# Kernel optimization log

Measured on AMD Instinct MI355X. Metric: run time of the kernel, lower is better.

The kernel has to match this reference:

```python
import jax, jax.numpy as jnp
import numpy as np

SCALE = 10.0
KB = 1.0  # kernel_bandwidth

B, D, P, M, K = 128, 128, 4, 100000, 10


def _sqdist(a, b):
    # a: [..., N, D], b: [..., M, D] -> squared euclidean [..., N, M]
    a2 = jnp.sum(a * a, axis=-1)[..., :, None]
    b2 = jnp.sum(b * b, axis=-1)[..., None, :]
    ab = jnp.einsum('...nd,...md->...nm', a, b)
    return jnp.maximum(a2 + b2 - 2.0 * ab, 0.0)


def setup_inputs() -> dict:
    key = jax.random.key(0)
    k1, k2, k3, k4, k5, k6, k7 = jax.random.split(key, 7)
    return {
        'global_img_feat': jax.random.normal(k1, (B, D), jnp.float32),
        'global_text_feat': jax.random.normal(k2, (B, D), jnp.float32),
        'local_img_feats': jax.random.normal(k3, (P, B, D), jnp.float32),
        'centers': jax.random.normal(k4, (P, M, D), jnp.float32),
        'cross_indices': jax.random.randint(k5, (B, K), 0, M, jnp.int64),
        'position': jax.random.randint(k6, (B,), 0, M, jnp.int64),
        'memory_vid': jax.random.randint(k7, (M,), 0, 1000, jnp.int64),
    }


def reference(global_img_feat, global_text_feat, local_img_feats, centers,
              cross_indices, position, memory_vid):
    b = global_img_feat.shape[0]
    # ---- global MMD alignment (text branch detached) ----
    img = global_img_feat / jnp.linalg.norm(global_img_feat, axis=1, keepdims=True)
    txt_d = jax.lax.stop_gradient(global_text_feat)
    txt = txt_d / jnp.linalg.norm(txt_d, axis=1, keepdims=True)
    inv2kb2 = 1.0 / (2.0 * KB * KB)
    k_xx = jnp.exp(-_sqdist(img, img) * inv2kb2)
    k_yy = jnp.exp(-_sqdist(txt, txt) * inv2kb2)
    k_xy = jnp.exp(-_sqdist(img, txt) * inv2kb2)
    off = ~jnp.eye(b, dtype=bool)
    denom = b * (b - 1)
    mmd = (jnp.sum(jnp.where(off, k_xx, 0.0)) / denom
           + jnp.sum(jnp.where(off, k_yy, 0.0)) / denom
           - 2.0 * jnp.mean(k_xy))
    # ---- local part contrastive loss (vectorized over P parts) ----
    m = centers.shape[1]
    pos_feat = centers[:, cross_indices]                       # [P,B,K,D]
    f2 = jnp.sum(local_img_feats ** 2, axis=-1)                # [P,B]
    p2 = jnp.sum(pos_feat ** 2, axis=-1)                       # [P,B,K]
    fp = jnp.einsum('pbd,pbkd->pbk', local_img_feats, pos_feat)
    pos_dist = jnp.sqrt(jnp.maximum(f2[..., None] + p2 - 2.0 * fp, 0.0))  # [P,B,K]
    neg_dist = jnp.sqrt(_sqdist(local_img_feats, centers))     # [P,B,M]
    # negative mask over memory slots (int indices are constants)
    neg_mask = jnp.ones((m,), bool).at[cross_indices.reshape(-1)].set(False)
    neg_mask = neg_mask.at[position].set(False)
    x = jnp.log(jnp.sum(jnp.exp(-SCALE * pos_dist), axis=-1))  # [P,B]
    y = jnp.log(jnp.sum(jnp.exp(-SCALE * neg_dist) * neg_mask[None, None, :], axis=-1))
    l = jnp.sum(-x + y, axis=1) / local_img_feats.shape[1]     # [P]
    l = jnp.where(jnp.isnan(l), 0.0, l)
    local_loss = jnp.sum(l) / local_img_feats.shape[0]
    total = local_loss + 1.0 * mmd
    pos_vid = memory_vid[cross_indices]                        # [B,K]
    return total, local_loss, mmd, pos_vid
```

## Files before the change

kernel.cpp:

```cpp
#include <hip/hip_runtime.h>
#include <math.h>

#define B_ 128
#define D_ 128
#define P_ 4
#define M_ 100000
#define K_ 10
#define SCALE_ 10.0f
#define MB_ 782
#define NEG_BLOCKS (MB_ * P_)
#define MMD_BLOCKS 128
#define POS_BLOCKS 128
#define D2_CUT 120.0f

typedef short bf16x8 __attribute__((ext_vector_type(8)));
typedef float floatx4 __attribute__((ext_vector_type(4)));

__device__ inline unsigned pack_bf16_trunc(unsigned f0, unsigned f1) {
    return __builtin_amdgcn_perm(f1, f0, 0x07060302u);
}

template <int CTRL>
__device__ inline float dpp_add(float v) {
    int x = __builtin_amdgcn_update_dpp(0, __builtin_bit_cast(int, v), CTRL, 0xF, 0xF, true);
    return v + __builtin_bit_cast(float, x);
}
__device__ inline float row16Sum(float v) {
    v = dpp_add<0xB1>(v);
    v = dpp_add<0x4E>(v);
    v = dpp_add<0x141>(v);
    v = dpp_add<0x140>(v);
    return v;
}
__device__ inline float waveSum64(float v) {
    v = row16Sum(v);
    v += __shfl_xor(v, 16, 64);
    v += __shfl_xor(v, 32, 64);
    return v;
}
__device__ inline float waveReduceSumOld(float v) {
    #pragma unroll
    for (int off = 32; off > 0; off >>= 1) v += __shfl_xor(v, off, 64);
    return v;
}
__device__ inline float blockReduce128(float v, float* sh2) {
    v = waveSum64(v);
    int wid = threadIdx.x >> 6;
    if ((threadIdx.x & 63) == 0) sh2[wid] = v;
    __syncthreads();
    float r = sh2[0] + sh2[1];
    __syncthreads();
    return r;
}

__global__ __launch_bounds__(128) void k_prep(const float* __restrict__ img,
                                              const float* __restrict__ txt,
                                              const float* __restrict__ local,
                                              float* imgT, float* txtT,
                                              float* a2i, float* a2t,
                                              float* f2w, float* s_neg) {
    __shared__ float sh2[2];
    int bid = blockIdx.x, t = threadIdx.x;
    if (bid < 256) {
        int row = bid & 127, which = bid >> 7;
        if (bid < 4) s_neg[bid * 128 + t] = 0.f;
        const float* src = which ? txt : img;
        float* dstT = which ? txtT : imgT;
        float* a2 = which ? a2t : a2i;
        float v = src[row * D_ + t];
        float s = blockReduce128(v * v, sh2);
        float n = v / sqrtf(s);
        dstT[t * 128 + row] = n;
        float s2 = blockReduce128(n * n, sh2);
        if (t == 0) a2[row] = s2;
    } else {
        int r = bid - 256;
        float v = local[(size_t)r * D_ + t];
        float s = blockReduce128(v * v, sh2);
        if (t == 0) f2w[r] = s;
    }
}

__global__ __launch_bounds__(256, 3) void k_main(const float* __restrict__ local,
                                                 const float* __restrict__ centers,
                                                 const float* __restrict__ imgT,
                                                 const float* __restrict__ txtT,
                                                 const float* __restrict__ a2i,
                                                 const float* __restrict__ a2t,
                                                 const int* __restrict__ ci,
                                                 const int* __restrict__ posi,
                                                 const int* __restrict__ mvid,
                                                 const float* __restrict__ f2w,
                                                 float* __restrict__ s_neg,
                                                 float* __restrict__ s_pos,
                                                 double* __restrict__ mmd_part,
                                                 float* __restrict__ out) {
    union Smem {
        struct {
            bf16x8 A_lds[2048];
            float sred[512];
            float f2l[128];
            unsigned char msk[128];
        } n;
        struct {
            float ri[128], rt[128];
            float sh2[2];
        } m;
    };
    __shared__ Smem sm;
    const int bid = blockIdx.x;
    const int t = threadIdx.x;
    const int w = t >> 6;
    const int l = t & 63;

    if (bid < NEG_BLOCKS) {
        const int p = bid / MB_;
        const int mb = bid - p * MB_;
        const int m0 = mb * 128;
        const int n16 = l & 15;
        const int q = l >> 4;

        const float* lp = local + (size_t)p * B_ * D_;
        if (t < 128) { sm.n.msk[t] = 1; sm.n.f2l[t] = f2w[p * 128 + t]; }
        #pragma unroll
        for (int s8 = 0; s8 < 8; s8++) {
            int f = t + 256 * s8;
            int fl = f & 63, bt = (f >> 6) & 7, kc = f >> 9;
            int row = bt * 16 + (fl & 15);
            int col = kc * 32 + ((fl >> 4) & 3) * 8;
            const uint4 u0 = *(const uint4*)(lp + row * D_ + col);
            const uint4 u1 = *(const uint4*)(lp + row * D_ + col + 4);
            union { bf16x8 v; unsigned u[4]; } fr;
            fr.u[0] = pack_bf16_trunc(u0.x, u0.y);
            fr.u[1] = pack_bf16_trunc(u0.z, u0.w);
            fr.u[2] = pack_bf16_trunc(u1.x, u1.y);
            fr.u[3] = pack_bf16_trunc(u1.z, u1.w);
            sm.n.A_lds[f] = fr.v;
        }
        __syncthreads();

        int gm[2];
        gm[0] = m0 + (w * 2 + 0) * 16 + n16;
        gm[1] = m0 + (w * 2 + 1) * 16 + n16;
        const float* cb = centers + (size_t)p * M_ * D_;
        uint4 rb[2][4][2];
        if (m0 + 128 <= M_) {
            #pragma unroll
            for (int wm = 0; wm < 2; wm++) {
                const uint4* src = (const uint4*)(cb + (size_t)gm[wm] * D_ + q * 8);
                #pragma unroll
                for (int kc = 0; kc < 4; kc++) {
                    rb[wm][kc][0] = src[kc * 8];
                    rb[wm][kc][1] = src[kc * 8 + 1];
                }
            }
        } else {
            const uint4 z = make_uint4(0u, 0u, 0u, 0u);
            #pragma unroll
            for (int wm = 0; wm < 2; wm++) {
                const uint4* src = (const uint4*)(cb + (size_t)gm[wm] * D_ + q * 8);
                #pragma unroll
                for (int kc = 0; kc < 4; kc++) {
                    if (gm[wm] < M_) {
                        rb[wm][kc][0] = src[kc * 8];
                        rb[wm][kc][1] = src[kc * 8 + 1];
                    } else {
                        rb[wm][kc][0] = z;
                        rb[wm][kc][1] = z;
                    }
                }
            }
        }

        #pragma unroll
        for (int i = 0; i < 5; i++) {
            int idx = ci[t + 256 * i];
            unsigned r = (unsigned)(idx - m0);
            if (r < 128u) sm.n.msk[r] = 0;
        }
        if (t < B_) {
            unsigned r = (unsigned)(posi[t] - m0);
            if (r < 128u) sm.n.msk[r] = 0;
        }
        __syncthreads();

        float c2a[2];
        bf16x8 bfr[2][4];
        #pragma unroll
        for (int wm = 0; wm < 2; wm++) {
            float c = 0.f;
            #pragma unroll
            for (int kc = 0; kc < 4; kc++) {
                union { uint4 u; floatx4 f; } a, b;
                a.u = rb[wm][kc][0];
                b.u = rb[wm][kc][1];
                c += a.f[0]*a.f[0] + a.f[1]*a.f[1] + a.f[2]*a.f[2] + a.f[3]*a.f[3]
                   + b.f[0]*b.f[0] + b.f[1]*b.f[1] + b.f[2]*b.f[2] + b.f[3]*b.f[3];
                union { bf16x8 v; unsigned u[4]; } fr;
                fr.u[0] = pack_bf16_trunc(a.u.x, a.u.y);
                fr.u[1] = pack_bf16_trunc(a.u.z, a.u.w);
                fr.u[2] = pack_bf16_trunc(b.u.x, b.u.y);
                fr.u[3] = pack_bf16_trunc(b.u.z, b.u.w);
                bfr[wm][kc] = fr.v;
            }
            c2a[wm] = c;
        }

        floatx4 acc[8][2];
        #pragma unroll
        for (int bt = 0; bt < 8; bt++) { acc[bt][0] = (floatx4)(0.f); acc[bt][1] = (floatx4)(0.f); }
        #pragma unroll
        for (int kc = 0; kc < 4; kc++) {
            #pragma unroll
            for (int bt = 0; bt < 8; bt++) {
                bf16x8 af = sm.n.A_lds[kc * 512 + bt * 64 + l];
                acc[bt][0] = __builtin_amdgcn_mfma_f32_16x16x32_bf16(af, bfr[0][kc], acc[bt][0], 0, 0, 0);
                acc[bt][1] = __builtin_amdgcn_mfma_f32_16x16x32_bf16(af, bfr[1][kc], acc[bt][1], 0, 0, 0);
            }
        }

        float c2v[2];
        #pragma unroll
        for (int wm = 0; wm < 2; wm++) {
            float c = c2a[wm];
            c += __shfl_xor(c, 16, 64);
            c += __shfl_xor(c, 32, 64);
            c2v[wm] = c;
        }

        float dmin = 1e30f;
        #pragma unroll
        for (int bt = 0; bt < 8; bt++) {
            floatx4 f4 = *(const floatx4*)&sm.n.f2l[bt * 16 + q * 4];
            #pragma unroll
            for (int r = 0; r < 4; r++) {
                float d20 = fmaf(-2.f, acc[bt][0][r], f4[r] + c2v[0]);
                float d21 = fmaf(-2.f, acc[bt][1][r], f4[r] + c2v[1]);
                dmin = fminf(dmin, fminf(d20, d21));
            }
        }
        if (!__any(dmin < D2_CUT)) {
            sm.n.sred[w * 128 + l] = 0.f;
            sm.n.sred[w * 128 + l + 64] = 0.f;
        } else {
            float vm0 = (gm[0] < M_ && sm.n.msk[(w * 2 + 0) * 16 + n16] != 0) ? 1.f : 0.f;
            float vm1 = (gm[1] < M_ && sm.n.msk[(w * 2 + 1) * 16 + n16] != 0) ? 1.f : 0.f;
            #pragma unroll
            for (int bt = 0; bt < 8; bt++) {
                floatx4 f4 = *(const floatx4*)&sm.n.f2l[bt * 16 + q * 4];
                #pragma unroll
                for (int r = 0; r < 4; r++) {
                    float s = 0.f;
                    float d20 = fmaxf(fmaf(-2.f, acc[bt][0][r], f4[r] + c2v[0]), 0.f);
                    float d21 = fmaxf(fmaf(-2.f, acc[bt][1][r], f4[r] + c2v[1]), 0.f);
                    if (d20 < D2_CUT) s += vm0 * expf(-SCALE_ * sqrtf(d20));
                    if (d21 < D2_CUT) s += vm1 * expf(-SCALE_ * sqrtf(d21));
                    s = row16Sum(s);
                    if (n16 == 0) sm.n.sred[w * 128 + bt * 16 + q * 4 + r] = s;
                }
            }
        }
        __syncthreads();
        if (t < 128) {
            float s = sm.n.sred[t] + sm.n.sred[128 + t] + sm.n.sred[256 + t] + sm.n.sred[384 + t];
            atomicAdd(&s_neg[p * 128 + t], s);
        }
    } else if (bid < NEG_BLOCKS + MMD_BLOCKS) {
        const int i = bid - NEG_BLOCKS;
        if (t < 128) {
            sm.m.ri[t] = imgT[t * 128 + i];
            sm.m.rt[t] = txtT[t * 128 + i];
        }
        __syncthreads();
        float kxx = 0.f, kyy = 0.f, kxy = 0.f;
        if (t < 128) {
            float dxx = 0.f, dyy = 0.f, dxy = 0.f;
            #pragma unroll 4
            for (int d = 0; d < D_; d++) {
                float rid = sm.m.ri[d], rtd = sm.m.rt[d];
                float av = imgT[d * 128 + t];
                float bv = txtT[d * 128 + t];
                dxx = fmaf(rid, av, dxx);
                dyy = fmaf(rtd, bv, dyy);
                dxy = fmaf(rid, bv, dxy);
            }
            kxx = (i == t) ? 0.f : expf(-fmaxf(a2i[i] + a2i[t] - 2.f * dxx, 0.f) * 0.5f);
            kyy = (i == t) ? 0.f : expf(-fmaxf(a2t[i] + a2t[t] - 2.f * dyy, 0.f) * 0.5f);
            kxy = expf(-fmaxf(a2i[i] + a2t[t] - 2.f * dxy, 0.f) * 0.5f);
        }
        float sxx = waveReduceSumOld(kxx);
        float syy = waveReduceSumOld(kyy);
        float sxy = waveReduceSumOld(kxy);
        __syncthreads();
        if (t == 0)  { sm.m.sh2[0] = sxx; }
        if (t == 64) { sm.m.sh2[1] = sxx; }
        __syncthreads();
        float txx = sm.m.sh2[0] + sm.m.sh2[1];
        __syncthreads();
        if (t == 0)  { sm.m.sh2[0] = syy; }
        if (t == 64) { sm.m.sh2[1] = syy; }
        __syncthreads();
        float tyy = sm.m.sh2[0] + sm.m.sh2[1];
        __syncthreads();
        if (t == 0)  { sm.m.sh2[0] = sxy; }
        if (t == 64) { sm.m.sh2[1] = sxy; }
        __syncthreads();
        float txy = sm.m.sh2[0] + sm.m.sh2[1];
        if (t == 0) {
            mmd_part[i] = (double)txx;
            mmd_part[128 + i] = (double)tyy;
            mmd_part[256 + i] = (double)txy;
        }
    } else {
        const int pair = (bid - (NEG_BLOCKS + MMD_BLOCKS)) * 4 + w;
        const int p = pair >> 7, b = pair & 127;
        const float* f = local + (size_t)pair * D_;
        float f0 = f[l], f1 = f[l + 64];
        float f2v = f2w[pair];
        const float* cb = centers + (size_t)p * M_ * D_;
        float s = 0.f;
        #pragma unroll
        for (int k = 0; k < K_; k++) {
            int idx = ci[b * K_ + k];
            const float* c = cb + (size_t)idx * D_;
            float c0 = c[l], c1 = c[l + 64];
            float p2 = waveSum64(c0 * c0 + c1 * c1);
            float fp = waveSum64(f0 * c0 + f1 * c1);
            float d2 = fmaxf(f2v + p2 - 2.f * fp, 0.f);
            if (d2 < D2_CUT) s += expf(-SCALE_ * sqrtf(d2));
        }
        if (l == 0) s_pos[pair] = s;
        if (p == 0 && l < K_) {
            int ix = ci[b * K_ + l];
            out[3 + b * K_ + l] = (float)mvid[ix];
        }
    }
}

__global__ __launch_bounds__(512) void k_final(const float* __restrict__ s_pos,
                                               const float* __restrict__ s_neg,
                                               const double* __restrict__ mmd_part,
                                               float* out) {
    __shared__ float red[512];
    __shared__ float lp_[4];
    int t = threadIdx.x;
    float x = logf(s_pos[t]);
    float y = logf(s_neg[t]);
    red[t] = -x + y;
    __syncthreads();
    for (int s = 64; s > 0; s >>= 1) {
        if ((t & 127) < s) red[t] += red[t + s];
        __syncthreads();
    }
    if ((t & 127) == 0) {
        float lv = red[t] / (float)B_;
        if (isnan(lv)) lv = 0.f;
        lp_[t >> 7] = lv;
    }
    __syncthreads();
    if (t == 0) {
        float local_loss = (lp_[0] + lp_[1] + lp_[2] + lp_[3]) / (float)P_;
        double sxx = 0.0, syy = 0.0, sxy = 0.0;
        for (int i = 0; i < 128; i++) {
            sxx += mmd_part[i];
            syy += mmd_part[128 + i];
            sxy += mmd_part[256 + i];
        }
        double denom = 128.0 * 127.0;
        float mmd = (float)(sxx / denom + syy / denom - 2.0 * (sxy / (128.0 * 128.0)));
        out[0] = local_loss + mmd;
        out[1] = local_loss;
        out[2] = mmd;
    }
}

extern "C" void kernel_launch(void* const* d_in, const int* in_sizes, int n_in,
                              void* d_out, int out_size, void* d_ws, size_t ws_size,
                              hipStream_t stream) {
    const float* img     = (const float*)d_in[0];
    const float* txt     = (const float*)d_in[1];
    const float* local   = (const float*)d_in[2];
    const float* centers = (const float*)d_in[3];
    const int*   ci      = (const int*)d_in[4];
    const int*   posi    = (const int*)d_in[5];
    const int*   mvid    = (const int*)d_in[6];
    float* out = (float*)d_out;

    char* ws = (char*)d_ws;
    float*  imgT     = (float*)(ws + 0);
    float*  txtT     = (float*)(ws + 65536);
    float*  a2i      = (float*)(ws + 131072);
    float*  a2t      = (float*)(ws + 131584);
    float*  f2w      = (float*)(ws + 132096);
    float*  s_pos    = (float*)(ws + 134144);
    float*  s_neg    = (float*)(ws + 136192);
    double* mmd_part = (double*)(ws + 138240);

    k_prep<<<768, 128, 0, stream>>>(img, txt, local, imgT, txtT, a2i, a2t, f2w, s_neg);
    k_main<<<NEG_BLOCKS + MMD_BLOCKS + POS_BLOCKS, 256, 0, stream>>>(
        local, centers, imgT, txtT, a2i, a2t, ci, posi, mvid, f2w,
        s_neg, s_pos, mmd_part, out);
    k_final<<<1, 512, 0, stream>>>(s_pos, s_neg, mmd_part, out);
}
```

Baseline: 329.5 us.

## Pre-pack bf16 A tiles in prep kernel and async-load them into LDS

The prep kernel now converts the local features to bf16 in MFMA fragment order once per part, and each negative block copies them straight into LDS with global_load_lds instead of reloading and repacking fp32 per block. The per-block negative mask in LDS is dropped: only blocks that pass the distance cutoff scan the cross and position indices directly. Occupancy is raised to 4 blocks per SM, and zero atomics are skipped. The cost is an extra prep phase and a serial 1408-iteration index scan in surviving blocks, which could be expensive if many blocks pass the cutoff.

```diff
diff --git a/kernel.cpp b/kernel.cpp
--- a/kernel.cpp
+++ b/kernel.cpp
@@ -58,7 +58,8 @@
                                               const float* __restrict__ local,
                                               float* imgT, float* txtT,
                                               float* a2i, float* a2t,
-                                              float* f2w, float* s_neg) {
+                                              float* f2w, float* s_neg,
+                                              bf16x8* __restrict__ Apk) {
     __shared__ float sh2[2];
     int bid = blockIdx.x, t = threadIdx.x;
     if (bid < 256) {
@@ -73,15 +74,30 @@
         dstT[t * 128 + row] = n;
         float s2 = blockReduce128(n * n, sh2);
         if (t == 0) a2[row] = s2;
-    } else {
+    } else if (bid < 768) {
         int r = bid - 256;
         float v = local[(size_t)r * D_ + t];
         float s = blockReduce128(v * v, sh2);
         if (t == 0) f2w[r] = s;
+    } else {
+        int g = (bid - 768) * 128 + t;
+        int p = g >> 11, f = g & 2047;
+        int fl = f & 63, bt = (f >> 6) & 7, kc = f >> 9;
+        int row = bt * 16 + (fl & 15);
+        int col = kc * 32 + ((fl >> 4) & 3) * 8;
+        const float* lp = local + (size_t)p * B_ * D_ + row * D_ + col;
+        const uint4 u0 = *(const uint4*)lp;
+        const uint4 u1 = *(const uint4*)(lp + 4);
+        union { bf16x8 v; unsigned u[4]; } fr;
+        fr.u[0] = pack_bf16_trunc(u0.x, u0.y);
+        fr.u[1] = pack_bf16_trunc(u0.z, u0.w);
+        fr.u[2] = pack_bf16_trunc(u1.x, u1.y);
+        fr.u[3] = pack_bf16_trunc(u1.z, u1.w);
+        Apk[g] = fr.v;
     }
 }
 
-__global__ __launch_bounds__(256, 3) void k_main(const float* __restrict__ local,
+__global__ __launch_bounds__(256, 4) void k_main(const float* __restrict__ local,
                                                  const float* __restrict__ centers,
                                                  const float* __restrict__ imgT,
                                                  const float* __restrict__ txtT,
@@ -91,6 +107,7 @@
                                                  const int* __restrict__ posi,
                                                  const int* __restrict__ mvid,
                                                  const float* __restrict__ f2w,
+                                                 const bf16x8* __restrict__ Apk,
                                                  float* __restrict__ s_neg,
                                                  float* __restrict__ s_pos,
                                                  double* __restrict__ mmd_part,
@@ -100,7 +117,6 @@
             bf16x8 A_lds[2048];
             float sred[512];
             float f2l[128];
-            unsigned char msk[128];
         } n;
         struct {
             float ri[128], rt[128];
@@ -119,25 +135,6 @@
         const int m0 = mb * 128;
         const int n16 = l & 15;
         const int q = l >> 4;
-
-        const float* lp = local + (size_t)p * B_ * D_;
-        if (t < 128) { sm.n.msk[t] = 1; sm.n.f2l[t] = f2w[p * 128 + t]; }
-        #pragma unroll
-        for (int s8 = 0; s8 < 8; s8++) {
-            int f = t + 256 * s8;
-            int fl = f & 63, bt = (f >> 6) & 7, kc = f >> 9;
-            int row = bt * 16 + (fl & 15);
-            int col = kc * 32 + ((fl >> 4) & 3) * 8;
-            const uint4 u0 = *(const uint4*)(lp + row * D_ + col);
-            const uint4 u1 = *(const uint4*)(lp + row * D_ + col + 4);
-            union { bf16x8 v; unsigned u[4]; } fr;
-            fr.u[0] = pack_bf16_trunc(u0.x, u0.y);
-            fr.u[1] = pack_bf16_trunc(u0.z, u0.w);
-            fr.u[2] = pack_bf16_trunc(u1.x, u1.y);
-            fr.u[3] = pack_bf16_trunc(u1.z, u1.w);
-            sm.n.A_lds[f] = fr.v;
-        }
-        __syncthreads();
 
         int gm[2];
         gm[0] = m0 + (w * 2 + 0) * 16 + n16;
@@ -172,17 +169,16 @@
             }
         }
 
-        #pragma unroll
-        for (int i = 0; i < 5; i++) {
-            int idx = ci[t + 256 * i];
-            unsigned r = (unsigned)(idx - m0);
-            if (r < 128u) sm.n.msk[r] = 0;
-        }
-        if (t < B_) {
-            unsigned r = (unsigned)(posi[t] - m0);
-            if (r < 128u) sm.n.msk[r] = 0;
-        }
-        __syncthreads();
+        const bf16x8* Ap = Apk + (p << 11);
+        #pragma unroll
+        for (int s8 = 0; s8 < 8; s8++) {
+            int fb = w * 64 + 256 * s8;
+            __builtin_amdgcn_global_load_lds(
+                (const __attribute__((address_space(1))) void*)(Ap + fb + l),
+                (__attribute__((address_space(3))) void*)(&sm.n.A_lds[fb]),
+                16, 0, 0);
+        }
+        if (t < 128) sm.n.f2l[t] = f2w[p * 128 + t];
 
         float c2a[2];
         bf16x8 bfr[2][4];
@@ -206,19 +202,6 @@
             c2a[wm] = c;
         }
 
-        floatx4 acc[8][2];
-        #pragma unroll
-        for (int bt = 0; bt < 8; bt++) { acc[bt][0] = (floatx4)(0.f); acc[bt][1] = (floatx4)(0.f); }
-        #pragma unroll
-        for (int kc = 0; kc < 4; kc++) {
-            #pragma unroll
-            for (int bt = 0; bt < 8; bt++) {
-                bf16x8 af = sm.n.A_lds[kc * 512 + bt * 64 + l];
-                acc[bt][0] = __builtin_amdgcn_mfma_f32_16x16x32_bf16(af, bfr[0][kc], acc[bt][0], 0, 0, 0);
-                acc[bt][1] = __builtin_amdgcn_mfma_f32_16x16x32_bf16(af, bfr[1][kc], acc[bt][1], 0, 0, 0);
-            }
-        }
-
         float c2v[2];
         #pragma unroll
         for (int wm = 0; wm < 2; wm++) {
@@ -228,6 +211,21 @@
             c2v[wm] = c;
         }
 
+        __syncthreads();
+
+        floatx4 acc[8][2];
+        #pragma unroll
+        for (int bt = 0; bt < 8; bt++) { acc[bt][0] = (floatx4)(0.f); acc[bt][1] = (floatx4)(0.f); }
+        #pragma unroll
+        for (int kc = 0; kc < 4; kc++) {
+            #pragma unroll
+            for (int bt = 0; bt < 8; bt++) {
+                bf16x8 af = sm.n.A_lds[kc * 512 + bt * 64 + l];
+                acc[bt][0] = __builtin_amdgcn_mfma_f32_16x16x32_bf16(af, bfr[0][kc], acc[bt][0], 0, 0, 0);
+                acc[bt][1] = __builtin_amdgcn_mfma_f32_16x16x32_bf16(af, bfr[1][kc], acc[bt][1], 0, 0, 0);
+            }
+        }
+
         float dmin = 1e30f;
         #pragma unroll
         for (int bt = 0; bt < 8; bt++) {
@@ -243,8 +241,18 @@
             sm.n.sred[w * 128 + l] = 0.f;
             sm.n.sred[w * 128 + l + 64] = 0.f;
         } else {
-            float vm0 = (gm[0] < M_ && sm.n.msk[(w * 2 + 0) * 16 + n16] != 0) ? 1.f : 0.f;
-            float vm1 = (gm[1] < M_ && sm.n.msk[(w * 2 + 1) * 16 + n16] != 0) ? 1.f : 0.f;
+            float vm0 = (gm[0] < M_) ? 1.f : 0.f;
+            float vm1 = (gm[1] < M_) ? 1.f : 0.f;
+            for (int i = 0; i < B_ * K_; i++) {
+                int idx = ci[i];
+                if (idx == gm[0]) vm0 = 0.f;
+                if (idx == gm[1]) vm1 = 0.f;
+            }
+            for (int i = 0; i < B_; i++) {
+                int idx = posi[i];
+                if (idx == gm[0]) vm0 = 0.f;
+                if (idx == gm[1]) vm1 = 0.f;
+            }
             #pragma unroll
             for (int bt = 0; bt < 8; bt++) {
                 floatx4 f4 = *(const floatx4*)&sm.n.f2l[bt * 16 + q * 4];
@@ -263,7 +271,7 @@
         __syncthreads();
         if (t < 128) {
             float s = sm.n.sred[t] + sm.n.sred[128 + t] + sm.n.sred[256 + t] + sm.n.sred[384 + t];
-            atomicAdd(&s_neg[p * 128 + t], s);
+            if (s != 0.f) atomicAdd(&s_neg[p * 128 + t], s);
         }
     } else if (bid < NEG_BLOCKS + MMD_BLOCKS) {
         const int i = bid - NEG_BLOCKS;
@@ -395,10 +403,11 @@
     float*  s_pos    = (float*)(ws + 134144);
     float*  s_neg    = (float*)(ws + 136192);
     double* mmd_part = (double*)(ws + 138240);
-
-    k_prep<<<768, 128, 0, stream>>>(img, txt, local, imgT, txtT, a2i, a2t, f2w, s_neg);
+    bf16x8* Apk      = (bf16x8*)(ws + 147456);
+
+    k_prep<<<832, 128, 0, stream>>>(img, txt, local, imgT, txtT, a2i, a2t, f2w, s_neg, Apk);
     k_main<<<NEG_BLOCKS + MMD_BLOCKS + POS_BLOCKS, 256, 0, stream>>>(
-        local, centers, imgT, txtT, a2i, a2t, ci, posi, mvid, f2w,
+        local, centers, imgT, txtT, a2i, a2t, ci, posi, mvid, f2w, Apk,
         s_neg, s_pos, mmd_part, out);
     k_final<<<1, 512, 0, stream>>>(s_pos, s_neg, mmd_part, out);
 }
```

Result: no change. 334.3 us (+1.5%).
